# Kernel optimization log

Hardware: AMD Instinct MI355X
Metric: run time of the kernel (lower is better)

The kernel has to match this reference:

```python
import jax, jax.numpy as jnp
import numpy as np

N_NODES = 100000
N_HEDGES = 100000
N_INC = 1000000
IN_DIM = 128
SEL_THRESHOLD = 0.5  # aug_node assumption: select nodes with low overlappness
EPS = 1e-10


def setup_inputs() -> dict:
    key = jax.random.key(0)
    ks = jax.random.split(key, 8)
    X = jax.random.normal(ks[0], (N_NODES, IN_DIM), dtype=jnp.float32)
    W1 = jax.random.normal(ks[1], (IN_DIM, IN_DIM // 2), dtype=jnp.float32) * 0.1
    b1 = jnp.zeros((IN_DIM // 2,), jnp.float32)
    W2 = jax.random.normal(ks[2], (IN_DIM // 2, 3), dtype=jnp.float32) * 0.1
    b2 = jnp.zeros((3,), jnp.float32)
    overlappness = jax.random.uniform(ks[3], (N_NODES,), dtype=jnp.float32)
    gumbel_u = jax.random.uniform(ks[4], (N_HEDGES, 3), dtype=jnp.float32)
    nodes = jax.random.randint(ks[5], (N_INC,), 0, N_NODES, dtype=jnp.int32)
    hedges = jax.random.randint(ks[6], (N_INC,), 0, N_HEDGES, dtype=jnp.int32)
    edge_index = jnp.stack([nodes, hedges], axis=0)
    return {"X": X, "W1": W1, "b1": b1, "W2": W2, "b2": b2,
            "overlappness": overlappness, "gumbel_u": gumbel_u,
            "edge_index": edge_index}


def _hypergraph_conv(X, ei0, ei1, W, b, n_nodes, n_hedges):
    # out = D^-1 H B^-1 H^T (X @ W) + b  (PyG HypergraphConv, unit edge weights)
    Xt = X @ W
    ones = jnp.ones((ei0.shape[0],), Xt.dtype)
    B = jax.ops.segment_sum(ones, ei1, num_segments=n_hedges)   # hyperedge degree
    D = jax.ops.segment_sum(ones, ei0, num_segments=n_nodes)    # node degree
    Binv = jnp.where(B > 0, 1.0 / B, 0.0)
    Dinv = jnp.where(D > 0, 1.0 / D, 0.0)
    Xe = jax.ops.segment_sum(Xt[ei0], ei1, num_segments=n_hedges) * Binv[:, None]
    Xn = jax.ops.segment_sum(Xe[ei1], ei0, num_segments=n_nodes) * Dinv[:, None]
    return Xn + b


def reference(X, W1, b1, W2, b2, overlappness, gumbel_u, edge_index):
    ei0 = edge_index[0]
    ei1 = edge_index[1]
    n_nodes = X.shape[0]
    n_hedges = gumbel_u.shape[0]

    # two-layer hypergraph encoder
    H1 = _hypergraph_conv(X, ei0, ei1, W1, b1, n_nodes, n_hedges)
    H2 = _hypergraph_conv(H1, ei0, ei1, W2, b2, n_nodes, n_hedges)  # [N, 3]

    # per-hyperedge scatter-mean of gathered node features
    ones = jnp.ones((ei0.shape[0],), H2.dtype)
    cnt = jax.ops.segment_sum(ones, ei1, num_segments=n_hedges)
    Xe = jax.ops.segment_sum(H2[ei0], ei1, num_segments=n_hedges)
    Xe = Xe * jnp.where(cnt > 0, 1.0 / cnt, 0.0)[:, None]

    # sigmoid + row-sum normalize (scale is detached in the original)
    Xe = jax.nn.sigmoid(Xe)
    rowsum = jax.lax.stop_gradient(jnp.sum(Xe, axis=1, keepdims=True))
    Xe = Xe * jnp.where(rowsum != 0, 1.0 / rowsum, 0.0)

    # gumbel-softmax (tau=1, hard) with explicit uniform noise
    g = -jnp.log(-jnp.log(gumbel_u + EPS) + EPS)
    y_soft = jax.nn.softmax(Xe + g, axis=-1)
    hard = jax.nn.one_hot(jnp.argmax(y_soft, axis=-1), 3, dtype=y_soft.dtype)

    sel_mask = (overlappness < SEL_THRESHOLD).astype(H2.dtype)  # aug_node
    reserve_f = hard[:, 0][ei1]                       # reserve edges
    mask_f = hard[:, 2][ei1] * sel_mask[ei0]          # masked-but-selected
    sample = jnp.maximum(reserve_f, mask_f)           # logical OR on {0,1}

    # jit-safe stand-in for edge_index[:, sample]: dropped columns -> -1
    keep = sample > 0
    edge_index_out = jnp.where(keep[None, :], edge_index, -1)
    return sample.astype(jnp.float32), edge_index_out
```

## Files before the change

kernel.cpp:

```cpp
#include <hip/hip_runtime.h>
#include <math.h>

#define N_NODES   100000
#define N_HEDGES  100000
#define N_INC     1000000
#define IN_DIM    128
#define SHIFT     7
#define BMASK     127
#define NBKT      782
#define CAP       2048
#define NBLK      245
#define BT        1024

typedef unsigned int u32;

__global__ void __launch_bounds__(BT)
build_kernel(const int* __restrict__ ei0, const int* __restrict__ ei1,
             const float* __restrict__ W1, const float* __restrict__ b1,
             const float* __restrict__ W2,
             int* __restrict__ gcur, u32* __restrict__ payload_n,
             u32* __restrict__ payload_h, float* __restrict__ W12,
             float* __restrict__ cvec)
{
    __shared__ int hA[NBKT], hB[NBKT];
    int blk = blockIdx.x, t = threadIdx.x;

    if (blk == 0) {
        if (t < 128) {
            float a0 = 0.f, a1 = 0.f, a2 = 0.f;
            for (int m = 0; m < 64; ++m) {
                float ww = W1[t * 64 + m];
                a0 += ww * W2[m * 3 + 0];
                a1 += ww * W2[m * 3 + 1];
                a2 += ww * W2[m * 3 + 2];
            }
            W12[t * 3 + 0] = a0; W12[t * 3 + 1] = a1; W12[t * 3 + 2] = a2;
        }
        if (t < 3) {
            float c = 0.f;
            for (int m = 0; m < 64; ++m) c += b1[m] * W2[m * 3 + t];
            cvec[t] = c;
        }
    }
    for (int i = t; i < NBKT; i += BT) { hA[i] = 0; hB[i] = 0; }
    __syncthreads();

    int i4 = blk * BT + t;
    bool ok = (i4 * 4 < N_INC);
    int4 n4 = ok ? ((const int4*)ei0)[i4] : make_int4(0, 0, 0, 0);
    int4 h4 = ok ? ((const int4*)ei1)[i4] : make_int4(0, 0, 0, 0);
    if (ok) {
        atomicAdd(&hA[n4.x >> SHIFT], 1); atomicAdd(&hB[h4.x >> SHIFT], 1);
        atomicAdd(&hA[n4.y >> SHIFT], 1); atomicAdd(&hB[h4.y >> SHIFT], 1);
        atomicAdd(&hA[n4.z >> SHIFT], 1); atomicAdd(&hB[h4.z >> SHIFT], 1);
        atomicAdd(&hA[n4.w >> SHIFT], 1); atomicAdd(&hB[h4.w >> SHIFT], 1);
    }
    __syncthreads();
    for (int i = t; i < NBKT; i += BT) {
        int c = hA[i];
        if (c) hA[i] = i * CAP + atomicAdd(&gcur[i * 16], c);
        c = hB[i];
        if (c) hB[i] = i * CAP + atomicAdd(&gcur[(NBKT + i) * 16], c);
    }
    __syncthreads();
    if (ok) {
        int nn[4] = {n4.x, n4.y, n4.z, n4.w};
        int hv[4] = {h4.x, h4.y, h4.z, h4.w};
        #pragma unroll
        for (int e = 0; e < 4; ++e) {
            int n = nn[e], h = hv[e];
            int pn = atomicAdd(&hA[n >> SHIFT], 1);
            int ph = atomicAdd(&hB[h >> SHIFT], 1);
            payload_n[pn] = ((u32)(n & BMASK) << 17) | (u32)h;
            payload_h[ph] = ((u32)(h & BMASK) << 17) | (u32)n;
        }
    }
}

__global__ void gemm_z_kernel(const float* __restrict__ X, const float* __restrict__ W12,
                              float* __restrict__ Z, int n_nodes) {
    __shared__ float w[IN_DIM * 3];
    int tid = threadIdx.x;
    for (int i = tid; i < IN_DIM * 3; i += blockDim.x) w[i] = W12[i];
    __syncthreads();

    int wave = tid >> 6;
    int lane = tid & 63;
    int half = lane >> 5, l = lane & 31;
    int node = (blockIdx.x * 4 + wave) * 2 + half;
    if (node >= n_nodes) return;

    float4 x4 = ((const float4*)(X + (size_t)node * IN_DIM))[l];
    int k = 4 * l;
    float a0 = x4.x * w[k*3+0] + x4.y * w[(k+1)*3+0] + x4.z * w[(k+2)*3+0] + x4.w * w[(k+3)*3+0];
    float a1 = x4.x * w[k*3+1] + x4.y * w[(k+1)*3+1] + x4.z * w[(k+2)*3+1] + x4.w * w[(k+3)*3+1];
    float a2 = x4.x * w[k*3+2] + x4.y * w[(k+1)*3+2] + x4.z * w[(k+2)*3+2] + x4.w * w[(k+3)*3+2];

    #pragma unroll
    for (int off = 16; off > 0; off >>= 1) {
        a0 += __shfl_xor(a0, off);
        a1 += __shfl_xor(a1, off);
        a2 += __shfl_xor(a2, off);
    }
    if (l == 0) {
        Z[(size_t)node * 4 + 0] = a0;
        Z[(size_t)node * 4 + 1] = a1;
        Z[(size_t)node * 4 + 2] = a2;
        Z[(size_t)node * 4 + 3] = 0.f;
    }
}

__global__ void __launch_bounds__(256)
phase2_kernel(const u32* __restrict__ payload_n, const u32* __restrict__ payload_h,
              const int* __restrict__ gcur,
              u32* __restrict__ od_n, u32* __restrict__ od_h,
              int* __restrict__ slot_n, int* __restrict__ slot_h)
{
    __shared__ int hist[128], curs[128];
    int t = threadIdx.x;
    int bk = blockIdx.x;
    int dir = (bk >= NBKT) ? 1 : 0;
    int b = bk - dir * NBKT;
    const u32* payload = dir ? payload_h : payload_n;
    u32* od   = dir ? od_h   : od_n;
    int* slot = dir ? slot_h : slot_n;
    int tot = gcur[bk * 16];
    int base = b * CAP;

    if (t < 128) hist[t] = 0;
    __syncthreads();
    for (int j = t; j < tot; j += 256) atomicAdd(&hist[payload[base + j] >> 17], 1);
    __syncthreads();
    if (t < 64) {
        int lane = t;
        int h0 = hist[lane], h1 = hist[64 + lane];
        int s0 = h0, s1 = h1;
        #pragma unroll
        for (int d = 1; d < 64; d <<= 1) {
            int u0 = __shfl_up(s0, d), u1 = __shfl_up(s1, d);
            if (lane >= d) { s0 += u0; s1 += u1; }
        }
        int tot0 = __shfl(s0, 63);
        int e0 = s0 - h0, e1 = tot0 + s1 - h1;
        int d0 = (b << SHIFT) + lane, d1 = d0 + 64;
        if (d0 < N_NODES) od[d0] = ((u32)(base + e0) << 10) | (u32)h0;
        if (d1 < N_NODES) od[d1] = ((u32)(base + e1) << 10) | (u32)h1;
        curs[lane] = e0; curs[64 + lane] = e1;
    }
    __syncthreads();
    for (int j = t; j < tot; j += 256) {
        u32 p = payload[base + j];
        int r = atomicAdd(&curs[p >> 17], 1);
        slot[base + r] = (int)(p & 0x1FFFF);
    }
}

__global__ void gather_kernel(const float* __restrict__ src, float* __restrict__ dst,
                              const u32* __restrict__ od, const int* __restrict__ slot,
                              const float* __restrict__ addv, int nrows) {
    int tid = blockIdx.x * blockDim.x + threadIdx.x;
    int r = tid >> 2, sub = tid & 3;
    if (r >= nrows) return;
    u32 v = od[r];
    int s = (int)(v >> 10), deg = (int)(v & 1023);
    float a0 = 0.f, a1 = 0.f, a2 = 0.f;
    for (int j = s + sub; j < s + deg; j += 4) {
        float4 x = ((const float4*)src)[slot[j]];
        a0 += x.x; a1 += x.y; a2 += x.z;
    }
    a0 += __shfl_xor(a0, 1); a1 += __shfl_xor(a1, 1); a2 += __shfl_xor(a2, 1);
    a0 += __shfl_xor(a0, 2); a1 += __shfl_xor(a1, 2); a2 += __shfl_xor(a2, 2);
    if (sub == 0) {
        float inv = deg > 0 ? 1.0f / (float)deg : 0.f;
        float b0 = 0.f, b1 = 0.f, b2 = 0.f;
        if (addv) { b0 = addv[0]; b1 = addv[1]; b2 = addv[2]; }
        ((float4*)dst)[r] = make_float4(a0 * inv + b0, a1 * inv + b1, a2 * inv + b2, 0.f);
    }
}

__global__ void hedge_final_kernel(const float* __restrict__ H2,
                                   const u32* __restrict__ od_h, const int* __restrict__ slot_h,
                                   const float* __restrict__ gu, float* __restrict__ hard0,
                                   float* __restrict__ hard2, int n) {
    int tid = blockIdx.x * blockDim.x + threadIdx.x;
    int h = tid >> 2, sub = tid & 3;
    if (h >= n) return;
    u32 v = od_h[h];
    int s = (int)(v >> 10), deg = (int)(v & 1023);
    float a0 = 0.f, a1 = 0.f, a2 = 0.f;
    for (int j = s + sub; j < s + deg; j += 4) {
        float4 x = ((const float4*)H2)[slot_h[j]];
        a0 += x.x; a1 += x.y; a2 += x.z;
    }
    a0 += __shfl_xor(a0, 1); a1 += __shfl_xor(a1, 1); a2 += __shfl_xor(a2, 1);
    a0 += __shfl_xor(a0, 2); a1 += __shfl_xor(a1, 2); a2 += __shfl_xor(a2, 2);
    if (sub != 0) return;
    float binv = deg > 0 ? 1.0f / (float)deg : 0.f;
    float s0 = a0 * binv, s1 = a1 * binv, s2 = a2 * binv;
    float x0 = 1.0f / (1.0f + expf(-s0));
    float x1 = 1.0f / (1.0f + expf(-s1));
    float x2 = 1.0f / (1.0f + expf(-s2));
    float rs = x0 + x1 + x2;
    float rinv = rs != 0.f ? 1.0f / rs : 0.f;
    x0 *= rinv; x1 *= rinv; x2 *= rinv;
    const float EPS = 1e-10f;
    float g0 = -logf(-logf(gu[(size_t)h * 3 + 0] + EPS) + EPS);
    float g1 = -logf(-logf(gu[(size_t)h * 3 + 1] + EPS) + EPS);
    float g2 = -logf(-logf(gu[(size_t)h * 3 + 2] + EPS) + EPS);
    float v0 = x0 + g0, v1 = x1 + g1, v2 = x2 + g2;
    int am = 0; float vm = v0;
    if (v1 > vm) { am = 1; vm = v1; }
    if (v2 > vm) { am = 2; vm = v2; }
    hard0[h] = (am == 0) ? 1.f : 0.f;
    hard2[h] = (am == 2) ? 1.f : 0.f;
}

__global__ void edge_final_kernel(const float* __restrict__ hard0, const float* __restrict__ hard2,
                                  const float* __restrict__ ov,
                                  const int* __restrict__ ei0, const int* __restrict__ ei1,
                                  float* __restrict__ out, int n4) {
    int i4 = blockIdx.x * blockDim.x + threadIdx.x;
    if (i4 >= n4) return;
    int4 n4v = ((const int4*)ei0)[i4];
    int4 h4v = ((const int4*)ei1)[i4];
    int nn[4] = {n4v.x, n4v.y, n4v.z, n4v.w};
    int hh[4] = {h4v.x, h4v.y, h4v.z, h4v.w};
    float smp[4], oi[4], oh[4];
    #pragma unroll
    for (int e = 0; e < 4; ++e) {
        float r = hard0[hh[e]];
        float m = hard2[hh[e]] * (ov[nn[e]] < 0.5f ? 1.f : 0.f);
        float s = fmaxf(r, m);
        smp[e] = s;
        bool keep = s > 0.f;
        oi[e] = keep ? (float)nn[e] : -1.f;
        oh[e] = keep ? (float)hh[e] : -1.f;
    }
    ((float4*)out)[i4] = make_float4(smp[0], smp[1], smp[2], smp[3]);
    ((float4*)(out + N_INC))[i4] = make_float4(oi[0], oi[1], oi[2], oi[3]);
    ((float4*)(out + 2 * (size_t)N_INC))[i4] = make_float4(oh[0], oh[1], oh[2], oh[3]);
}

extern "C" void kernel_launch(void* const* d_in, const int* in_sizes, int n_in,
                              void* d_out, int out_size, void* d_ws, size_t ws_size,
                              hipStream_t stream) {
    const float* X  = (const float*)d_in[0];
    const float* W1 = (const float*)d_in[1];
    const float* b1 = (const float*)d_in[2];
    const float* W2 = (const float*)d_in[3];
    const float* b2 = (const float*)d_in[4];
    const float* ov = (const float*)d_in[5];
    const float* gu = (const float*)d_in[6];
    const int*   ei = (const int*)d_in[7];
    const int* ei0 = ei;
    const int* ei1 = ei + N_INC;

    int* ip = (int*)d_ws;
    int* gcur      = ip;
    u32* payload_n = (u32*)(gcur + 25024);
    u32* payload_h = payload_n + NBKT * CAP;
    int* slot_n    = (int*)(payload_h + NBKT * CAP);
    int* slot_h    = slot_n + NBKT * CAP;
    u32* od_n      = (u32*)(slot_h + NBKT * CAP);
    u32* od_h      = od_n + 100096;
    float* W12     = (float*)(od_h + 100096);
    float* cvec    = W12 + 384;
    float* Z       = cvec + 16;
    float* XeA     = Z    + 4 * N_NODES;
    float* XnA     = XeA  + 4 * N_HEDGES;
    float* XeB     = XnA  + 4 * N_NODES;
    float* XnB     = XeB  + 4 * N_HEDGES;
    float* hard0   = XnB  + 4 * N_NODES;
    float* hard2   = hard0 + N_HEDGES;

    const int TB = 256;
    int gQuad = (4 * N_NODES + TB - 1) / TB;

    hipMemsetAsync(gcur, 0, 25024 * sizeof(int), stream);

    build_kernel<<<NBLK, BT, 0, stream>>>(ei0, ei1, W1, b1, W2,
                                          gcur, payload_n, payload_h, W12, cvec);
    gemm_z_kernel<<<(N_NODES + 7) / 8, 256, 0, stream>>>(X, W12, Z, N_NODES);
    phase2_kernel<<<2 * NBKT, 256, 0, stream>>>(payload_n, payload_h, gcur,
                                                od_n, od_h, slot_n, slot_h);

    gather_kernel<<<gQuad, TB, 0, stream>>>(Z,   XeA, od_h, slot_h, nullptr, N_HEDGES);
    gather_kernel<<<gQuad, TB, 0, stream>>>(XeA, XnA, od_n, slot_n, cvec,    N_NODES);
    gather_kernel<<<gQuad, TB, 0, stream>>>(XnA, XeB, od_h, slot_h, nullptr, N_HEDGES);
    gather_kernel<<<gQuad, TB, 0, stream>>>(XeB, XnB, od_n, slot_n, b2,      N_NODES);

    hedge_final_kernel<<<gQuad, TB, 0, stream>>>(XnB, od_h, slot_h, gu, hard0, hard2, N_HEDGES);

    edge_final_kernel<<<(N_INC / 4 + TB - 1) / TB, TB, 0, stream>>>(hard0, hard2, ov, ei0, ei1,
                                                                    (float*)d_out, N_INC / 4);
}
```

Measured before the change: 128.1 us.

## Fuse bucketing with Z GEMM, replace memset, widen gather to 8 lanes/row

```diff
diff --git a/kernel.cpp b/kernel.cpp
--- a/kernel.cpp
+++ b/kernel.cpp
@@ -10,21 +10,16 @@
 #define NBKT      782
 #define CAP       2048
 #define NBLK      245
+#define GEMM_BLKS 3125
 #define BT        1024
 
 typedef unsigned int u32;
 
-__global__ void __launch_bounds__(BT)
-build_kernel(const int* __restrict__ ei0, const int* __restrict__ ei1,
-             const float* __restrict__ W1, const float* __restrict__ b1,
-             const float* __restrict__ W2,
-             int* __restrict__ gcur, u32* __restrict__ payload_n,
-             u32* __restrict__ payload_h, float* __restrict__ W12,
-             float* __restrict__ cvec)
-{
-    __shared__ int hA[NBKT], hB[NBKT];
+__global__ void __launch_bounds__(256)
+init_kernel(const float* __restrict__ W1, const float* __restrict__ b1,
+            const float* __restrict__ W2, float* __restrict__ W12,
+            float* __restrict__ cvec, int* __restrict__ gcur) {
     int blk = blockIdx.x, t = threadIdx.x;
-
     if (blk == 0) {
         if (t < 128) {
             float a0 = 0.f, a1 = 0.f, a2 = 0.f;
@@ -41,72 +36,79 @@
             for (int m = 0; m < 64; ++m) c += b1[m] * W2[m * 3 + t];
             cvec[t] = c;
         }
-    }
-    for (int i = t; i < NBKT; i += BT) { hA[i] = 0; hB[i] = 0; }
-    __syncthreads();
-
-    int i4 = blk * BT + t;
-    bool ok = (i4 * 4 < N_INC);
-    int4 n4 = ok ? ((const int4*)ei0)[i4] : make_int4(0, 0, 0, 0);
-    int4 h4 = ok ? ((const int4*)ei1)[i4] : make_int4(0, 0, 0, 0);
-    if (ok) {
-        atomicAdd(&hA[n4.x >> SHIFT], 1); atomicAdd(&hB[h4.x >> SHIFT], 1);
-        atomicAdd(&hA[n4.y >> SHIFT], 1); atomicAdd(&hB[h4.y >> SHIFT], 1);
-        atomicAdd(&hA[n4.z >> SHIFT], 1); atomicAdd(&hB[h4.z >> SHIFT], 1);
-        atomicAdd(&hA[n4.w >> SHIFT], 1); atomicAdd(&hB[h4.w >> SHIFT], 1);
-    }
-    __syncthreads();
-    for (int i = t; i < NBKT; i += BT) {
-        int c = hA[i];
-        if (c) hA[i] = i * CAP + atomicAdd(&gcur[i * 16], c);
-        c = hB[i];
-        if (c) hB[i] = i * CAP + atomicAdd(&gcur[(NBKT + i) * 16], c);
-    }
-    __syncthreads();
-    if (ok) {
+    } else {
+        int i = (blk - 1) * 256 + t;
+        if (i < 25024) gcur[i] = 0;
+    }
+}
+
+__global__ void __launch_bounds__(BT)
+fused_kernel(const int* __restrict__ ei0, const int* __restrict__ ei1,
+             const float* __restrict__ X, const float* __restrict__ W12,
+             int* __restrict__ gcur, u32* __restrict__ payload_n,
+             u32* __restrict__ payload_h, float* __restrict__ Z)
+{
+    __shared__ int hA[NBKT], hB[NBKT];
+    __shared__ float w[IN_DIM * 3];
+    int blk = blockIdx.x, t = threadIdx.x;
+
+    if (blk < NBLK) {
+        for (int i = t; i < NBKT; i += BT) { hA[i] = 0; hB[i] = 0; }
+        __syncthreads();
+        int i4 = blk * BT + t;
+        bool ok = (i4 * 4 < N_INC);
+        int4 n4 = ok ? ((const int4*)ei0)[i4] : make_int4(0, 0, 0, 0);
+        int4 h4 = ok ? ((const int4*)ei1)[i4] : make_int4(0, 0, 0, 0);
         int nn[4] = {n4.x, n4.y, n4.z, n4.w};
         int hv[4] = {h4.x, h4.y, h4.z, h4.w};
+        int rn[4], rh[4];
+        if (ok) {
+            #pragma unroll
+            for (int e = 0; e < 4; ++e) {
+                rn[e] = atomicAdd(&hA[nn[e] >> SHIFT], 1);
+                rh[e] = atomicAdd(&hB[hv[e] >> SHIFT], 1);
+            }
+        }
+        __syncthreads();
+        for (int i = t; i < NBKT; i += BT) {
+            int c = hA[i];
+            if (c) hA[i] = i * CAP + atomicAdd(&gcur[i * 16], c);
+            c = hB[i];
+            if (c) hB[i] = i * CAP + atomicAdd(&gcur[(NBKT + i) * 16], c);
+        }
+        __syncthreads();
+        if (ok) {
+            #pragma unroll
+            for (int e = 0; e < 4; ++e) {
+                int n = nn[e], h = hv[e];
+                payload_n[hA[n >> SHIFT] + rn[e]] = ((u32)(n & BMASK) << 17) | (u32)h;
+                payload_h[hB[h >> SHIFT] + rh[e]] = ((u32)(h & BMASK) << 17) | (u32)n;
+            }
+        }
+    } else {
+        for (int i = t; i < IN_DIM * 3; i += BT) w[i] = W12[i];
+        __syncthreads();
+        int wave = t >> 6, lane = t & 63;
+        int half = lane >> 5, l = lane & 31;
+        int node = (blk - NBLK) * 32 + wave * 2 + half;
+        if (node >= N_NODES) return;
+        float4 x4 = ((const float4*)(X + (size_t)node * IN_DIM))[l];
+        int k = 4 * l;
+        float a0 = x4.x*w[k*3+0] + x4.y*w[(k+1)*3+0] + x4.z*w[(k+2)*3+0] + x4.w*w[(k+3)*3+0];
+        float a1 = x4.x*w[k*3+1] + x4.y*w[(k+1)*3+1] + x4.z*w[(k+2)*3+1] + x4.w*w[(k+3)*3+1];
+        float a2 = x4.x*w[k*3+2] + x4.y*w[(k+1)*3+2] + x4.z*w[(k+2)*3+2] + x4.w*w[(k+3)*3+2];
         #pragma unroll
-        for (int e = 0; e < 4; ++e) {
-            int n = nn[e], h = hv[e];
-            int pn = atomicAdd(&hA[n >> SHIFT], 1);
-            int ph = atomicAdd(&hB[h >> SHIFT], 1);
-            payload_n[pn] = ((u32)(n & BMASK) << 17) | (u32)h;
-            payload_h[ph] = ((u32)(h & BMASK) << 17) | (u32)n;
-        }
-    }
-}
-
-__global__ void gemm_z_kernel(const float* __restrict__ X, const float* __restrict__ W12,
-                              float* __restrict__ Z, int n_nodes) {
-    __shared__ float w[IN_DIM * 3];
-    int tid = threadIdx.x;
-    for (int i = tid; i < IN_DIM * 3; i += blockDim.x) w[i] = W12[i];
-    __syncthreads();
-
-    int wave = tid >> 6;
-    int lane = tid & 63;
-    int half = lane >> 5, l = lane & 31;
-    int node = (blockIdx.x * 4 + wave) * 2 + half;
-    if (node >= n_nodes) return;
-
-    float4 x4 = ((const float4*)(X + (size_t)node * IN_DIM))[l];
-    int k = 4 * l;
-    float a0 = x4.x * w[k*3+0] + x4.y * w[(k+1)*3+0] + x4.z * w[(k+2)*3+0] + x4.w * w[(k+3)*3+0];
-    float a1 = x4.x * w[k*3+1] + x4.y * w[(k+1)*3+1] + x4.z * w[(k+2)*3+1] + x4.w * w[(k+3)*3+1];
-    float a2 = x4.x * w[k*3+2] + x4.y * w[(k+1)*3+2] + x4.z * w[(k+2)*3+2] + x4.w * w[(k+3)*3+2];
-
-    #pragma unroll
-    for (int off = 16; off > 0; off >>= 1) {
-        a0 += __shfl_xor(a0, off);
-        a1 += __shfl_xor(a1, off);
-        a2 += __shfl_xor(a2, off);
-    }
-    if (l == 0) {
-        Z[(size_t)node * 4 + 0] = a0;
-        Z[(size_t)node * 4 + 1] = a1;
-        Z[(size_t)node * 4 + 2] = a2;
-        Z[(size_t)node * 4 + 3] = 0.f;
+        for (int off = 16; off > 0; off >>= 1) {
+            a0 += __shfl_xor(a0, off);
+            a1 += __shfl_xor(a1, off);
+            a2 += __shfl_xor(a2, off);
+        }
+        if (l == 0) {
+            Z[(size_t)node * 4 + 0] = a0;
+            Z[(size_t)node * 4 + 1] = a1;
+            Z[(size_t)node * 4 + 2] = a2;
+            Z[(size_t)node * 4 + 3] = 0.f;
+        }
     }
 }
 
@@ -159,17 +161,18 @@
                               const u32* __restrict__ od, const int* __restrict__ slot,
                               const float* __restrict__ addv, int nrows) {
     int tid = blockIdx.x * blockDim.x + threadIdx.x;
-    int r = tid >> 2, sub = tid & 3;
+    int r = tid >> 3, sub = tid & 7;
     if (r >= nrows) return;
     u32 v = od[r];
     int s = (int)(v >> 10), deg = (int)(v & 1023);
     float a0 = 0.f, a1 = 0.f, a2 = 0.f;
-    for (int j = s + sub; j < s + deg; j += 4) {
+    for (int j = s + sub; j < s + deg; j += 8) {
         float4 x = ((const float4*)src)[slot[j]];
         a0 += x.x; a1 += x.y; a2 += x.z;
     }
     a0 += __shfl_xor(a0, 1); a1 += __shfl_xor(a1, 1); a2 += __shfl_xor(a2, 1);
     a0 += __shfl_xor(a0, 2); a1 += __shfl_xor(a1, 2); a2 += __shfl_xor(a2, 2);
+    a0 += __shfl_xor(a0, 4); a1 += __shfl_xor(a1, 4); a2 += __shfl_xor(a2, 4);
     if (sub == 0) {
         float inv = deg > 0 ? 1.0f / (float)deg : 0.f;
         float b0 = 0.f, b1 = 0.f, b2 = 0.f;
@@ -274,20 +277,19 @@
     float* hard2   = hard0 + N_HEDGES;
 
     const int TB = 256;
+    int gOct  = (8 * N_NODES + TB - 1) / TB;
     int gQuad = (4 * N_NODES + TB - 1) / TB;
 
-    hipMemsetAsync(gcur, 0, 25024 * sizeof(int), stream);
-
-    build_kernel<<<NBLK, BT, 0, stream>>>(ei0, ei1, W1, b1, W2,
-                                          gcur, payload_n, payload_h, W12, cvec);
-    gemm_z_kernel<<<(N_NODES + 7) / 8, 256, 0, stream>>>(X, W12, Z, N_NODES);
+    init_kernel<<<99, 256, 0, stream>>>(W1, b1, W2, W12, cvec, gcur);
+    fused_kernel<<<NBLK + GEMM_BLKS, BT, 0, stream>>>(ei0, ei1, X, W12, gcur,
+                                                      payload_n, payload_h, Z);
     phase2_kernel<<<2 * NBKT, 256, 0, stream>>>(payload_n, payload_h, gcur,
                                                 od_n, od_h, slot_n, slot_h);
 
-    gather_kernel<<<gQuad, TB, 0, stream>>>(Z,   XeA, od_h, slot_h, nullptr, N_HEDGES);
-    gather_kernel<<<gQuad, TB, 0, stream>>>(XeA, XnA, od_n, slot_n, cvec,    N_NODES);
-    gather_kernel<<<gQuad, TB, 0, stream>>>(XnA, XeB, od_h, slot_h, nullptr, N_HEDGES);
-    gather_kernel<<<gQuad, TB, 0, stream>>>(XeB, XnB, od_n, slot_n, b2,      N_NODES);
+    gather_kernel<<<gOct, TB, 0, stream>>>(Z,   XeA, od_h, slot_h, nullptr, N_HEDGES);
+    gather_kernel<<<gOct, TB, 0, stream>>>(XeA, XnA, od_n, slot_n, cvec,    N_NODES);
+    gather_kernel<<<gOct, TB, 0, stream>>>(XnA, XeB, od_h, slot_h, nullptr, N_HEDGES);
+    gather_kernel<<<gOct, TB, 0, stream>>>(XeB, XnB, od_n, slot_n, b2,      N_NODES);
 
     hedge_final_kernel<<<gQuad, TB, 0, stream>>>(XnB, od_h, slot_h, gu, hard0, hard2, N_HEDGES);
 
```

After: 129.7 us. No clear change (+1.2%).
